# Performance work log

Measured on AMD Instinct MI355X. Metric: run time of the kernel, lower is better.

## Reference

```python
import jax, jax.numpy as jnp
import numpy as np

N = 100000      # nodes
E = 1600000     # edges (avg degree 16)
D_IN = 128
D_OUT = 128
ALPHA = 0.2     # leaky-relu negative slope
EPS = 1e-8


def setup_inputs() -> dict:
    key = jax.random.key(0)
    kx, kr, kc, kW, ka = jax.random.split(key, 5)
    x = jax.random.normal(kx, (N, D_IN), dtype=jnp.float32)
    row = jax.random.randint(kr, (E,), 0, N)
    col = jax.random.randint(kc, (E,), 0, N)
    stdv_w = 1.0 / np.sqrt(D_OUT)
    W = jax.random.uniform(kW, (D_IN, D_OUT), jnp.float32, -stdv_w, stdv_w)
    stdv_a = 1.0 / np.sqrt(2 * D_OUT)
    a = jax.random.uniform(ka, (2 * D_OUT, 1), jnp.float32, -stdv_a, stdv_a)
    return {"x": x, "row": row, "col": col, "W": W, "a": a}


def reference(x, row, col, W, a):
    # h = x W : [N, D_OUT]
    h = x @ W
    n = x.shape[0]
    # a is applied to cat([h_row, h_col]); split so we never materialize [E, 2*D_OUT]:
    # e_ij = leaky_relu(h_i . a[:D] + h_j . a[D:])
    s_src = h @ a[:D_OUT, 0]   # [N]
    s_dst = h @ a[D_OUT:, 0]   # [N]
    e = s_src[row] + s_dst[col]               # [E]
    e = jnp.where(e > 0, e, ALPHA * e)        # leaky relu
    # segment (per-row) softmax, numerically stable
    row_max = jax.ops.segment_max(e, row, num_segments=n)
    e_exp = jnp.exp(e - row_max[row])
    row_sum = jax.ops.segment_sum(e_exp, row, num_segments=n)
    row_sum = jnp.maximum(row_sum, EPS)       # clamp(min=1e-8)
    att = e_exp / row_sum[row]                # [E]
    # sparse.mm(attention, h): scatter-add of att * h[col] into rows
    h_prime = jax.ops.segment_sum(att[:, None] * h[col], row, num_segments=n)
    # concat=True -> elu
    return jax.nn.elu(h_prime)
```

## Files before the change

kernel.cpp:

```cpp
#include <hip/hip_runtime.h>
#include <cstddef>

#define ALPHA 0.2f
#define EPS 1e-8f
#define LOG_RPB 6
#define RPB 64
#define COL_BITS 17
#define COL_MASK 0x1FFFFu
#define CAP 2048
#define SCHUNK 8192
#define MAXCHUNK 256

typedef __attribute__((ext_vector_type(8))) short short8v;
typedef __attribute__((ext_vector_type(4))) float f32x4;

static __device__ __forceinline__ unsigned short f2bf(float f) {
  unsigned int u = __float_as_uint(f);
  unsigned int r = u + 0x7fffu + ((u >> 16) & 1u);
  return (unsigned short)(r >> 16);
}
static __device__ __forceinline__ float bf2f(unsigned short s) {
  return __uint_as_float(((unsigned int)s) << 16);
}

__global__ __launch_bounds__(256) void wt_prep_kernel(
    const float* __restrict__ W, unsigned short* __restrict__ wt) {
  int idx = blockIdx.x * 256 + threadIdx.x;
  int nn = idx >> 7, k = idx & 127;
  wt[idx] = f2bf(W[k * 128 + nn]);
}

__global__ __launch_bounds__(512) void gemm_sort_kernel(
    const float* __restrict__ x, const unsigned short* __restrict__ wt,
    const float* __restrict__ a, const int* __restrict__ row,
    const int* __restrict__ col, unsigned short* __restrict__ h_bf,
    float* __restrict__ s_src, float* __restrict__ s_dst,
    unsigned int* __restrict__ chunk_sorted, int* __restrict__ scanarr,
    int n, int E, int nbin_pad, int nchunk) {
  extern __shared__ char smem[];
  const int t = threadIdx.x;
  const int wave = t >> 6, lane = t & 63;

  if ((int)blockIdx.x < nchunk) {
    unsigned int* sorted = (unsigned int*)smem;
    int* hist = (int*)(smem + SCHUNK * 4);
    int* wsum = (int*)(smem + SCHUNK * 4 + (size_t)nbin_pad * 4);
    const int ci = blockIdx.x;
    const int e0 = ci * SCHUNK;
    const int eend = (e0 + SCHUNK < E) ? e0 + SCHUNK : E;
    const int m = eend - e0;

    for (int b = t; b < nbin_pad; b += 512) hist[b] = 0;
    __syncthreads();
    for (int i = e0 + t * 4; i < eend; i += 2048) {
      if (i + 3 < eend) {
        int4 v = *(const int4*)&row[i];
        atomicAdd(&hist[v.x >> LOG_RPB], 1);
        atomicAdd(&hist[v.y >> LOG_RPB], 1);
        atomicAdd(&hist[v.z >> LOG_RPB], 1);
        atomicAdd(&hist[v.w >> LOG_RPB], 1);
      } else {
        for (int j = 0; j < 4 && i + j < eend; j++)
          atomicAdd(&hist[row[i + j] >> LOG_RPB], 1);
      }
    }
    __syncthreads();

    int v[4];
    int lsum = 0;
#pragma unroll
    for (int j = 0; j < 4; j++) {
      int idx = t * 4 + j;
      v[j] = (idx < nbin_pad) ? hist[idx] : 0;
      lsum += v[j];
    }
    int incl = lsum;
#pragma unroll
    for (int off = 1; off < 64; off <<= 1) {
      int y = __shfl_up(incl, off, 64);
      if (lane >= off) incl += y;
    }
    if (lane == 63) wsum[wave] = incl;
    __syncthreads();
    if (t < 8) {
      int wv = wsum[t];
      int wincl = wv;
#pragma unroll
      for (int off = 1; off < 8; off <<= 1) {
        int y = __shfl_up(wincl, off, 64);
        if (t >= off) wincl += y;
      }
      wsum[t] = wincl - wv;
    }
    __syncthreads();
    int base = wsum[wave] + incl - lsum;
#pragma unroll
    for (int j = 0; j < 4; j++) {
      int idx = t * 4 + j;
      if (idx < nbin_pad) hist[idx] = base;
      base += v[j];
    }
    __syncthreads();

    int* sa = scanarr + (size_t)ci * nbin_pad;
    for (int b = t; b < nbin_pad; b += 512) sa[b] = hist[b];
    __syncthreads();

    for (int i = e0 + t; i < eend; i += 512) {
      int r = row[i], c = col[i];
      int b = r >> LOG_RPB;
      int pos = atomicAdd(&hist[b], 1);
      sorted[pos] = ((unsigned int)(r & (RPB - 1)) << COL_BITS) |
                    ((unsigned int)c & COL_MASK);
    }
    __syncthreads();

    {
      int i = t * 4;
      for (; i + 3 < m; i += 2048)
        *(uint4*)&chunk_sorted[(size_t)e0 + i] = *(const uint4*)&sorted[i];
      for (int k = (m & ~3) + t; k < m; k += 512)
        chunk_sorted[(size_t)e0 + k] = sorted[k];
    }
    return;
  }

  const int gb = blockIdx.x - nchunk;
  unsigned short* c_lds = (unsigned short*)smem;
  const int n16 = lane & 15, g = lane >> 4;
  const int row0 = gb * 128 + wave * 16;
  int arow = row0 + n16;
  if (arow >= n) arow = n - 1;

  f32x4 acc[8];
#pragma unroll
  for (int cf = 0; cf < 8; cf++) acc[cf] = (f32x4){0.f, 0.f, 0.f, 0.f};

#pragma unroll
  for (int s = 0; s < 4; s++) {
    const int k0 = s * 32 + g * 8;
    const float* xr = x + (size_t)arow * 128 + k0;
    float4 av0 = ((const float4*)xr)[0];
    float4 av1 = ((const float4*)xr)[1];
    short8v afrag;
    afrag[0] = (short)f2bf(av0.x); afrag[1] = (short)f2bf(av0.y);
    afrag[2] = (short)f2bf(av0.z); afrag[3] = (short)f2bf(av0.w);
    afrag[4] = (short)f2bf(av1.x); afrag[5] = (short)f2bf(av1.y);
    afrag[6] = (short)f2bf(av1.z); afrag[7] = (short)f2bf(av1.w);
#pragma unroll
    for (int cf = 0; cf < 8; cf++) {
      short8v bfrag = *(const short8v*)(wt + (size_t)(cf * 16 + n16) * 128 + k0);
      acc[cf] = __builtin_amdgcn_mfma_f32_16x16x32_bf16(afrag, bfrag, acc[cf], 0, 0, 0);
    }
  }

  float p0[4] = {0.f, 0.f, 0.f, 0.f}, p1[4] = {0.f, 0.f, 0.f, 0.f};
#pragma unroll
  for (int cf = 0; cf < 8; cf++) {
    const int colx = cf * 16 + n16;
    const float a0 = a[colx], a1 = a[128 + colx];
#pragma unroll
    for (int j = 0; j < 4; j++) {
      float v = acc[cf][j];
      c_lds[(wave * 16 + g * 4 + j) * 128 + colx] = f2bf(v);
      p0[j] += v * a0;
      p1[j] += v * a1;
    }
  }
#pragma unroll
  for (int j = 0; j < 4; j++) {
#pragma unroll
    for (int off = 1; off <= 8; off <<= 1) {
      p0[j] += __shfl_xor(p0[j], off, 64);
      p1[j] += __shfl_xor(p1[j], off, 64);
    }
  }
  if (n16 == 0) {
#pragma unroll
    for (int j = 0; j < 4; j++) {
      int r = row0 + g * 4 + j;
      if (r < n) { s_src[r] = p0[j]; s_dst[r] = p1[j]; }
    }
  }
  __syncthreads();
  {
    int rw = t >> 2, q = t & 3;
    int nid = gb * 128 + rw;
    if (nid < n) {
      const uint4* src = (const uint4*)&c_lds[rw * 128 + q * 32];
      uint4 v0 = src[0], v1 = src[1], v2 = src[2], v3 = src[3];
      uint4* dst = (uint4*)&h_bf[(size_t)nid * 128 + q * 32];
      dst[0] = v0; dst[1] = v1; dst[2] = v2; dst[3] = v3;
    }
  }
}

__global__ __launch_bounds__(512) void attend_bin_kernel(
    const unsigned short* __restrict__ h_bf,
    const unsigned int* __restrict__ chunk_sorted,
    const int* __restrict__ scanarr, const float* __restrict__ s_src,
    const float* __restrict__ s_dst, float* __restrict__ out,
    int n, int nbin_pad, int nchunk) {
  __shared__ uint2 ep[CAP];
  __shared__ unsigned int ep_raw[CAP];
  __shared__ float s_row[RPB];
  __shared__ int hist[RPB];
  __shared__ int cursor[RPB];
  __shared__ int rowbase[RPB + 1];
  __shared__ int segoff[MAXCHUNK + 1];
  __shared__ int segsrc[MAXCHUNK];
  __shared__ int s_tot;

  const int bin = blockIdx.x;
  const int t = threadIdx.x;
  const int wave = t >> 6;
  const int lane = t & 63;

  int cnt_c = 0, s0 = 0;
  if (t < nchunk) {
    const int* sa = scanarr + (size_t)t * nbin_pad;
    s0 = sa[bin];
    cnt_c = sa[bin + 1] - s0;
  }
  if (t < MAXCHUNK) { segoff[t] = cnt_c; segsrc[t] = s0; }
  if (t < RPB) {
    hist[t] = 0;
    int r = (bin << LOG_RPB) + t;
    s_row[t] = (r < n) ? s_src[r] : 0.f;
  }
  __syncthreads();

  if (wave == 0) {
    int carry = 0;
#pragma unroll
    for (int gq = 0; gq < MAXCHUNK / 64; gq++) {
      int idx = gq * 64 + lane;
      int vv = segoff[idx];
      int inc = vv;
#pragma unroll
      for (int off = 1; off < 64; off <<= 1) {
        int y = __shfl_up(inc, off, 64);
        if (lane >= off) inc += y;
      }
      segoff[idx] = inc - vv + carry;
      carry += __shfl(inc, 63, 64);
    }
    if (lane == 0) { s_tot = carry; segoff[MAXCHUNK] = carry; }
  }
  __syncthreads();
  const int cnt = s_tot < CAP ? s_tot : CAP;

  for (int i = t; i < cnt; i += 512) {
    int lo = 0, hi = nchunk;
    while (hi - lo > 1) {
      int mid = (lo + hi) >> 1;
      if (segoff[mid] <= i) lo = mid; else hi = mid;
    }
    unsigned int u = chunk_sorted[(size_t)lo * SCHUNK + segsrc[lo] + (i - segoff[lo])];
    ep_raw[i] = u;
    atomicAdd(&hist[u >> COL_BITS], 1);
  }
  __syncthreads();

  if (wave == 0) {
    int orig = hist[lane];
    int v = orig;
#pragma unroll
    for (int off = 1; off < 64; off <<= 1) {
      int y = __shfl_up(v, off, 64);
      if (lane >= off) v += y;
    }
    rowbase[lane + 1] = v;
    cursor[lane] = v - orig;
    if (lane == 0) rowbase[0] = 0;
  }
  __syncthreads();

  for (int i = t; i < cnt; i += 512) {
    unsigned int u = ep_raw[i];
    int lr = (int)(u >> COL_BITS);
    int c = (int)(u & COL_MASK);
    float ev = s_row[lr] + s_dst[c];
    ev = ev > 0.f ? ev : ALPHA * ev;
    float p = __expf(ev);
    int pos = atomicAdd(&cursor[lr], 1);
    ep[pos] = make_uint2((unsigned int)c << 8, __float_as_uint(p));
  }
  __syncthreads();

  const char* hlane = (const char*)h_bf + (size_t)(lane << 2);
  for (int rr = 0; rr < 8; ++rr) {
    const int lr = wave * 8 + rr;
    const int r = (bin << LOG_RPB) + lr;
    if (r >= n) continue;
    const int rs = rowbase[lr];
    const int deg = rowbase[lr + 1] - rs;
    float acc0 = 0.f, acc1 = 0.f, ssum = 0.f;

    int k = 0;
    for (; k + 16 <= deg; k += 16) {
      uint2 e[16];
      ushort2 v[16];
#pragma unroll
      for (int i = 0; i < 16; i++) e[i] = ep[rs + k + i];
#pragma unroll
      for (int i = 0; i < 16; i++)
        v[i] = *(const ushort2*)(hlane + e[i].x);
#pragma unroll
      for (int i = 0; i < 16; i++) {
        float p = __uint_as_float(e[i].y);
        ssum += p;
        acc0 += p * bf2f(v[i].x);
        acc1 += p * bf2f(v[i].y);
      }
    }
    for (; k + 4 <= deg; k += 4) {
      uint2 e[4];
      ushort2 v[4];
#pragma unroll
      for (int i = 0; i < 4; i++) e[i] = ep[rs + k + i];
#pragma unroll
      for (int i = 0; i < 4; i++)
        v[i] = *(const ushort2*)(hlane + e[i].x);
#pragma unroll
      for (int i = 0; i < 4; i++) {
        float p = __uint_as_float(e[i].y);
        ssum += p;
        acc0 += p * bf2f(v[i].x);
        acc1 += p * bf2f(v[i].y);
      }
    }
    for (; k < deg; ++k) {
      uint2 e = ep[rs + k];
      ushort2 v = *(const ushort2*)(hlane + e.x);
      float p = __uint_as_float(e.y);
      ssum += p;
      acc0 += p * bf2f(v.x);
      acc1 += p * bf2f(v.y);
    }

    float inv = 1.0f / fmaxf(ssum, EPS);
    acc0 *= inv; acc1 *= inv;
    float o0 = acc0 > 0.f ? acc0 : expm1f(acc0);
    float o1 = acc1 > 0.f ? acc1 : expm1f(acc1);
    *(float2*)&out[(size_t)r * 128 + lane * 2] = make_float2(o0, o1);
  }
}

static inline size_t align256(size_t v) { return (v + 255) & ~(size_t)255; }

extern "C" void kernel_launch(void* const* d_in, const int* in_sizes, int n_in,
                              void* d_out, int out_size, void* d_ws, size_t ws_size,
                              hipStream_t stream) {
  const float* x   = (const float*)d_in[0];
  const int*   row = (const int*)d_in[1];
  const int*   col = (const int*)d_in[2];
  const float* W   = (const float*)d_in[3];
  const float* a   = (const float*)d_in[4];
  float* out = (float*)d_out;

  const int N = in_sizes[0] / 128;
  const int E = in_sizes[1];
  const int NBIN = (N + RPB - 1) >> LOG_RPB;
  const int NBIN_PAD = (NBIN + 16) & ~15;
  const int NCHUNK = (E + SCHUNK - 1) / SCHUNK;
  const int NBG = (N + 127) / 128;

  char* ws = (char*)d_ws;
  unsigned short* h_bf = (unsigned short*)ws; ws += align256((size_t)N * 128 * 2);
  unsigned short* wt   = (unsigned short*)ws; ws += align256((size_t)128 * 128 * 2);
  float* s_src = (float*)ws;          ws += align256((size_t)N * 4);
  float* s_dst = (float*)ws;          ws += align256((size_t)N * 4);
  unsigned int* chunk_sorted = (unsigned int*)ws;
  ws += align256((size_t)NCHUNK * SCHUNK * 4);
  int* scanarr = (int*)ws;            ws += align256((size_t)NCHUNK * NBIN_PAD * 4);

  const size_t lds_bytes = (size_t)SCHUNK * 4 + (size_t)NBIN_PAD * 4 + 64;

  wt_prep_kernel<<<dim3(64), dim3(256), 0, stream>>>(W, wt);
  gemm_sort_kernel<<<dim3(NCHUNK + NBG), dim3(512), lds_bytes, stream>>>(
      x, wt, a, row, col, h_bf, s_src, s_dst, chunk_sorted, scanarr,
      N, E, NBIN_PAD, NCHUNK);
  attend_bin_kernel<<<dim3(NBIN), dim3(512), 0, stream>>>(
      h_bf, chunk_sorted, scanarr, s_src, s_dst, out, N, NBIN_PAD, NCHUNK);
}
```

Before: 130.0 us.

## Process two row bins per attention block with 1024 threads

The attention kernel now handles two adjacent 64-row bins per block, using 1024 threads and doubled LDS capacity for edges. The per-chunk split point between the two bins, read from the scan array, tags each edge with a local row index from 0 to 127. Merging bins halves the number of blocks, so the per-block setup (scan-array reads, segment prefix scan, binary-search metadata) is paid half as often. In exchange each block uses more LDS and has a larger footprint, which may reduce how many blocks fit on a CU and leave load less evenly spread across CUs.

```diff
diff --git a/kernel.cpp b/kernel.cpp
--- a/kernel.cpp
+++ b/kernel.cpp
@@ -7,7 +7,7 @@
 #define RPB 64
 #define COL_BITS 17
 #define COL_MASK 0x1FFFFu
-#define CAP 2048
+#define CAP 4096
 #define SCHUNK 8192
 #define MAXCHUNK 256
 
@@ -195,7 +195,7 @@
   }
 }
 
-__global__ __launch_bounds__(512) void attend_bin_kernel(
+__global__ __launch_bounds__(1024) void attend_bin_kernel(
     const unsigned short* __restrict__ h_bf,
     const unsigned int* __restrict__ chunk_sorted,
     const int* __restrict__ scanarr, const float* __restrict__ s_src,
@@ -203,29 +203,31 @@
     int n, int nbin_pad, int nchunk) {
   __shared__ uint2 ep[CAP];
   __shared__ unsigned int ep_raw[CAP];
-  __shared__ float s_row[RPB];
-  __shared__ int hist[RPB];
-  __shared__ int cursor[RPB];
-  __shared__ int rowbase[RPB + 1];
+  __shared__ float s_row[2 * RPB];
+  __shared__ int hist[2 * RPB];
+  __shared__ int cursor[2 * RPB];
+  __shared__ int rowbase[2 * RPB + 1];
   __shared__ int segoff[MAXCHUNK + 1];
   __shared__ int segsrc[MAXCHUNK];
+  __shared__ int segmid[MAXCHUNK];
   __shared__ int s_tot;
 
-  const int bin = blockIdx.x;
+  const int bin0 = blockIdx.x * 2;
   const int t = threadIdx.x;
   const int wave = t >> 6;
   const int lane = t & 63;
 
-  int cnt_c = 0, s0 = 0;
+  int cnt_c = 0, s0 = 0, mid = 0;
   if (t < nchunk) {
     const int* sa = scanarr + (size_t)t * nbin_pad;
-    s0 = sa[bin];
-    cnt_c = sa[bin + 1] - s0;
-  }
-  if (t < MAXCHUNK) { segoff[t] = cnt_c; segsrc[t] = s0; }
-  if (t < RPB) {
+    s0 = sa[bin0];
+    mid = sa[bin0 + 1] - s0;
+    cnt_c = sa[bin0 + 2] - s0;
+  }
+  if (t < MAXCHUNK) { segoff[t] = cnt_c; segsrc[t] = s0; segmid[t] = mid; }
+  if (t < 2 * RPB) {
     hist[t] = 0;
-    int r = (bin << LOG_RPB) + t;
+    int r = (bin0 << LOG_RPB) + t;
     s_row[t] = (r < n) ? s_src[r] : 0.f;
   }
   __syncthreads();
@@ -250,33 +252,41 @@
   __syncthreads();
   const int cnt = s_tot < CAP ? s_tot : CAP;
 
-  for (int i = t; i < cnt; i += 512) {
+  for (int i = t; i < cnt; i += 1024) {
     int lo = 0, hi = nchunk;
     while (hi - lo > 1) {
-      int mid = (lo + hi) >> 1;
-      if (segoff[mid] <= i) lo = mid; else hi = mid;
-    }
-    unsigned int u = chunk_sorted[(size_t)lo * SCHUNK + segsrc[lo] + (i - segoff[lo])];
-    ep_raw[i] = u;
-    atomicAdd(&hist[u >> COL_BITS], 1);
+      int mid2 = (lo + hi) >> 1;
+      if (segoff[mid2] <= i) lo = mid2; else hi = mid2;
+    }
+    int o = i - segoff[lo];
+    unsigned int u = chunk_sorted[(size_t)lo * SCHUNK + segsrc[lo] + o];
+    int lr = (int)(u >> COL_BITS) + ((o >= segmid[lo]) ? RPB : 0);
+    ep_raw[i] = (u & COL_MASK) | ((unsigned int)lr << COL_BITS);
+    atomicAdd(&hist[lr], 1);
   }
   __syncthreads();
 
   if (wave == 0) {
-    int orig = hist[lane];
-    int v = orig;
-#pragma unroll
-    for (int off = 1; off < 64; off <<= 1) {
-      int y = __shfl_up(v, off, 64);
-      if (lane >= off) v += y;
-    }
-    rowbase[lane + 1] = v;
-    cursor[lane] = v - orig;
+    int carry = 0;
+#pragma unroll
+    for (int gq = 0; gq < 2; gq++) {
+      int idx = gq * 64 + lane;
+      int orig = hist[idx];
+      int v = orig;
+#pragma unroll
+      for (int off = 1; off < 64; off <<= 1) {
+        int y = __shfl_up(v, off, 64);
+        if (lane >= off) v += y;
+      }
+      rowbase[idx + 1] = v + carry;
+      cursor[idx] = v - orig + carry;
+      carry += __shfl(v, 63, 64);
+    }
     if (lane == 0) rowbase[0] = 0;
   }
   __syncthreads();
 
-  for (int i = t; i < cnt; i += 512) {
+  for (int i = t; i < cnt; i += 1024) {
     unsigned int u = ep_raw[i];
     int lr = (int)(u >> COL_BITS);
     int c = (int)(u & COL_MASK);
@@ -291,7 +301,7 @@
   const char* hlane = (const char*)h_bf + (size_t)(lane << 2);
   for (int rr = 0; rr < 8; ++rr) {
     const int lr = wave * 8 + rr;
-    const int r = (bin << LOG_RPB) + lr;
+    const int r = (bin0 << LOG_RPB) + lr;
     if (r >= n) continue;
     const int rs = rowbase[lr];
     const int deg = rowbase[lr + 1] - rs;
@@ -365,6 +375,7 @@
   const int NBIN_PAD = (NBIN + 16) & ~15;
   const int NCHUNK = (E + SCHUNK - 1) / SCHUNK;
   const int NBG = (N + 127) / 128;
+  const int NPAIR = (NBIN + 1) / 2;
 
   char* ws = (char*)d_ws;
   unsigned short* h_bf = (unsigned short*)ws; ws += align256((size_t)N * 128 * 2);
@@ -381,6 +392,6 @@
   gemm_sort_kernel<<<dim3(NCHUNK + NBG), dim3(512), lds_bytes, stream>>>(
       x, wt, a, row, col, h_bf, s_src, s_dst, chunk_sorted, scanarr,
       N, E, NBIN_PAD, NCHUNK);
-  attend_bin_kernel<<<dim3(NBIN), dim3(512), 0, stream>>>(
+  attend_bin_kernel<<<dim3(NPAIR), dim3(1024), 0, stream>>>(
       h_bf, chunk_sorted, scanarr, s_src, s_dst, out, N, NBIN_PAD, NCHUNK);
 }
```

After: 152.1 us. +17.0%, slower.
